# Optimization experiments

Hardware: AMD Instinct MI355X
Metric: run time of the kernel (lower is better)

## Reference

```python
import jax, jax.numpy as jnp
import numpy as np

FTYPE = ((0, 16), (1, 16), (2, 8))   # [(order, multiplicity)], C = 16*1 + 16*2 + 8*2 = 64
DIM = 64
MAX_ORDER = 2
NUM_BASIS = 2 * MAX_ORDER + 1        # [1, cos a, sin a, cos 2a, sin 2a]
V = 50000
E = 800000
LN_EPS = 1e-5


def _transport(features, transporters, ftype):
    """Apply per-irrep rotation rho_n(g) to each edge's gathered feature. features:(E,C)."""
    blocks = []
    offset = 0
    for order, mult in ftype:
        d = 1 if order == 0 else 2
        C = mult * d
        blk = features[:, offset:offset + C]
        if order == 0:
            blocks.append(blk)
        else:
            b = blk.reshape(-1, mult, 2)                      # (E, mult, 2)
            phi = order * transporters
            c, s = jnp.cos(phi), jnp.sin(phi)
            R = jnp.stack([jnp.stack([c, -s], -1),
                           jnp.stack([s,  c], -1)], -2)        # (E, 2, 2)
            rot = jnp.einsum('emd,erd->emr', b, R)             # rotate each 2-vector
            blocks.append(rot.reshape(-1, C))
        offset += C
    return jnp.concatenate(blocks, axis=1)


def _angle_basis(angles):
    """Circular harmonic basis for the equivariant kernel: (E, NUM_BASIS)."""
    cols = [jnp.ones_like(angles)]
    for k in range(1, MAX_ORDER + 1):
        cols.append(jnp.cos(k * angles))
        cols.append(jnp.sin(k * angles))
    return jnp.stack(cols, axis=1)


def _regular_nonlin(x, ftype):
    """ReLU on scalar (rho_0) channels; norm-gated softplus on vector channels."""
    blocks = []
    offset = 0
    for order, mult in ftype:
        d = 1 if order == 0 else 2
        C = mult * d
        blk = x[:, offset:offset + C]
        if order == 0:
            blocks.append(jax.nn.relu(blk))
        else:
            b = blk.reshape(-1, mult, 2)
            norms = jnp.clip(jnp.linalg.norm(b, axis=-1, keepdims=True), 1e-8, None)
            out_b = b * (jax.nn.softplus(norms) / norms)
            blocks.append(out_b.reshape(-1, C))
        offset += C
    return jnp.concatenate(blocks, axis=1)


def _gem_block(x, edge_index, angles, transporters, K_self, W_neigh, ln_gamma, ln_beta):
    src, tgt = edge_index[0], edge_index[1]
    # self-interaction
    out = x @ K_self.T                                        # (V, C_out)
    # gather + parallel transport
    f_q = _transport(x[src], transporters, FTYPE)             # (E, C_in)
    # per-edge equivariant kernel applied via fused einsum:
    #   K_neigh[e] = sum_b basis[e,b] * W_neigh[b]  ;  msg[e] = K_neigh[e] @ f_q[e]
    basis = _angle_basis(angles)                              # (E, B)
    tmp = jnp.einsum('boi,ei->ebo', W_neigh, f_q)             # (E, B, C_out)
    msg = jnp.einsum('eb,ebo->eo', basis, tmp)                # (E, C_out)
    # scatter-add messages into targets
    out = out + jax.ops.segment_sum(msg, tgt, num_segments=V)
    # LayerNorm
    mu = jnp.mean(out, axis=-1, keepdims=True)
    var = jnp.var(out, axis=-1, keepdims=True)
    h = (out - mu) * jax.lax.rsqrt(var + LN_EPS) * ln_gamma + ln_beta
    # regular nonlinearity + identity residual (dim_in == dim_out)
    h = _regular_nonlin(h, FTYPE)
    return h + x


def setup_inputs() -> dict:
    key = jax.random.key(0)
    ks = jax.random.split(key, 8)
    x = jax.random.normal(ks[0], (V, DIM), jnp.float32)
    edge_index = jax.random.randint(ks[1], (2, E), 0, V)
    angles = jax.random.uniform(ks[2], (E,), jnp.float32, 0.0, 2.0 * np.pi)
    transporters = jax.random.uniform(ks[3], (E,), jnp.float32, 0.0, 2.0 * np.pi)
    K_self = jax.random.normal(ks[4], (DIM, DIM), jnp.float32) / np.sqrt(DIM)
    W_neigh = jax.random.normal(ks[5], (NUM_BASIS, DIM, DIM), jnp.float32) / np.sqrt(DIM * NUM_BASIS)
    ln_gamma = jnp.ones((DIM,), jnp.float32)
    ln_beta = jnp.zeros((DIM,), jnp.float32)
    return {"x": x, "edge_index": edge_index, "angles": angles, "transporters": transporters,
            "K_self": K_self, "W_neigh": W_neigh, "ln_gamma": ln_gamma, "ln_beta": ln_beta}


def reference(x, edge_index, angles, transporters, K_self, W_neigh, ln_gamma, ln_beta):
    return _gem_block(x, edge_index, angles, transporters, K_self, W_neigh, ln_gamma, ln_beta)
```

## Files before the change

kernel.cpp:

```cpp
#include <hip/hip_runtime.h>

#define VN 50000
#define EN 800000
#define CAP 48
#define USH 392

typedef short short8 __attribute__((ext_vector_type(8)));
typedef float float4v __attribute__((ext_vector_type(4)));

#define WS_GBF   0
#define WS_WHI   128
#define WS_WLO   12416
#define WS_POS   24704
#define WS_REC   74704
#define WS_A_BYTES ((size_t)(74704 + 50000 * 48 * 4) * 4)

__device__ __forceinline__ float bf2f(unsigned short u) {
    return __uint_as_float(((unsigned int)u) << 16);
}
__device__ __forceinline__ unsigned short f2bf(float f) {
    unsigned int x = __float_as_uint(f);
    return (unsigned short)((x + 0x7fffu + ((x >> 16) & 1u)) >> 16);
}
__device__ __forceinline__ float ldf(const void* p, int isbf, size_t i) {
    return isbf ? bf2f(((const unsigned short*)p)[i]) : ((const float*)p)[i];
}

__device__ __forceinline__ int block_detect(const void* xv) {
    __shared__ int flg;
    if (threadIdx.x < 64) {
        unsigned short w = ((const unsigned short*)xv)[2 * threadIdx.x];
        int e = (w >> 7) & 0xFF;
        bool ok = (e >= 0x70 && e <= 0x85) || (w == 0);
        unsigned long long m = __ballot(ok);
        if (threadIdx.x == 0) flg = (__popcll(m) >= 40) ? 1 : 0;
    }
    __syncthreads();
    return flg;
}

__device__ __forceinline__ void convert_dev(int idx, const void* Ks,
                                            const void* Wn, const void* gma,
                                            const void* bta, float* ws, int isbf) {
    if (idx < 128) {
        const void* p = (idx < 64) ? gma : bta;
        ws[WS_GBF + idx] = ldf(p, isbf, idx & 63);
    } else {
        int m2 = idx - 128;
        int j = m2 & 7;
        int chunk = m2 >> 3;
        int slot = chunk >> 6;
        int ln = chunk & 63;
        int ks = slot >> 2, wv = slot & 3;
        int k = ks * 32 + ((ln >> 4) * 8) + j;
        int n = wv * 16 + (ln & 15);
        float wvl;
        if (k < 320) {
            int b = k >> 6, i = k & 63;
            wvl = ldf(Wn, isbf, (b * 64 + n) * 64 + i);
        } else {
            wvl = ldf(Ks, isbf, n * 64 + (k - 320));
        }
        unsigned short hi = f2bf(wvl);
        unsigned short lo = f2bf(wvl - bf2f(hi));
        ((unsigned short*)(ws + WS_WHI))[m2] = hi;
        ((unsigned short*)(ws + WS_WLO))[m2] = lo;
    }
}

template <bool PAY>
__global__ __launch_bounds__(512) void conv_place(
    const void* xv, const int* __restrict__ eidx, const void* angv,
    const void* trpv, const void* Ks, const void* Wn, const void* gma,
    const void* bta, float* __restrict__ ws) {
    const int isbf = block_detect(xv);
    int gtid = blockIdx.x * 512 + threadIdx.x;
    if (gtid < 128 + 24576) convert_dev(gtid, Ks, Wn, gma, bta, ws, isbf);
    if (gtid < EN) {
        int tgt = eidx[EN + gtid];
        int slot = atomicAdd(&((int*)(ws + WS_POS))[tgt], 1);
        if (slot < CAP) {
            if (PAY) {
                uint4 r;
                r.x = (unsigned int)eidx[gtid];
                r.y = __float_as_uint(ldf(angv, isbf, gtid));
                r.z = __float_as_uint(ldf(trpv, isbf, gtid));
                r.w = 0u;
                ((uint4*)(ws + WS_REC))[(size_t)tgt * CAP + slot] = r;
            } else {
                ((int*)(ws + WS_REC))[(size_t)tgt * CAP + slot] = gtid;
            }
        }
    }
}

template <bool BF, bool PAY>
__device__ __forceinline__ void gem_body(
    const void* xv, const int* __restrict__ eidx, const void* angv,
    const void* trpv, const float* __restrict__ ws, void* __restrict__ outv,
    float* Ledge, unsigned short* Uhi, unsigned short* Ulo) {
    const int t = threadIdx.x;
    const int lane = t & 63;
    const int w = t >> 6;
    const int v0 = blockIdx.x * 8;
    const int* pos = (const int*)(ws + WS_POS);
    float* Cst = Ledge;

    if (t < 8 * CAP) {
        int n = t / CAP, s = t - n * CAP;
        int dn = min(pos[v0 + n], CAP);
        if (s < dn) {
            unsigned int srcb;
            float aphi, tphi;
            if (PAY) {
                uint4 r = ((const uint4*)(ws + WS_REC))[(size_t)(v0 + n) * CAP + s];
                srcb = r.x;
                aphi = __uint_as_float(r.y);
                tphi = __uint_as_float(r.z);
            } else {
                int e = ((const int*)(ws + WS_REC))[(size_t)(v0 + n) * CAP + s];
                srcb = (unsigned int)eidx[e];
                aphi = BF ? bf2f(((const unsigned short*)angv)[e])
                          : ((const float*)angv)[e];
                tphi = BF ? bf2f(((const unsigned short*)trpv)[e])
                          : ((const float*)trpv)[e];
            }
            float st, ct, sa, ca;
            __sincosf(tphi, &st, &ct);
            __sincosf(aphi, &sa, &ca);
            float c2a = fmaf(ca, ca, -sa * sa), s2a = 2.f * ca * sa;
            float c2t = fmaf(ct, ct, -st * st), s2t = 2.f * ct * st;
            float* L = &Ledge[t * 16];
            *(float4v*)(L)      = (float4v){__uint_as_float(srcb), ca, sa, c2a};
            *(float4v*)(L + 4)  = (float4v){1.f, 0.f, s2a, 0.f};
            *(float4v*)(L + 8)  = (float4v){ct, st, s2a, 0.f};
            *(float4v*)(L + 12) = (float4v){c2t, s2t, s2a, 0.f};
        }
    }
    __syncthreads();

    const int v = v0 + w;
    const int d = min(pos[v], CAP);
    const int g = (lane < 16) ? 0 : ((lane < 48) ? 1 : 2);
    const int grpoff = 4 + 4 * g;
    const unsigned int smask = (lane & 1) ? 0u : 0x80000000u;
    float a0 = 0.f, a1 = 0.f, a2 = 0.f, a3 = 0.f, a4 = 0.f;

    const float* Lb = &Ledge[w * CAP * 16];
    auto loadx = [&](unsigned int s) -> float {
        if (BF) return bf2f(((const unsigned short*)xv)[(size_t)s * 64 + lane]);
        else    return ((const float*)xv)[(size_t)s * 64 + lane];
    };
    auto edge1 = [&](int j, float xg) {
        const float* L = &Lb[j * 16];
        float4v sh = *(const float4v*)L;
        float4v gr = *(const float4v*)(L + grpoff);
        float prt = __shfl_xor(xg, 1, 64);
        float tmp = __uint_as_float(__float_as_uint(gr[1] * prt) ^ smask);
        float fq = fmaf(gr[0], xg, tmp);
        a0 += fq;
        a1 = fmaf(sh[1], fq, a1);
        a2 = fmaf(sh[2], fq, a2);
        a3 = fmaf(sh[3], fq, a3);
        a4 = fmaf(gr[2], fq, a4);
    };

    const int nb = d >> 2;
    float y0, y1, y2, y3;
    if (nb > 0) {
        y0 = loadx(__float_as_uint(Lb[0 * 16]));
        y1 = loadx(__float_as_uint(Lb[1 * 16]));
        y2 = loadx(__float_as_uint(Lb[2 * 16]));
        y3 = loadx(__float_as_uint(Lb[3 * 16]));
    }
    for (int b = 0; b < nb; ++b) {
        float z0, z1, z2, z3;
        const bool more = (b + 1 < nb);
        if (more) {
            int j4 = (b + 1) * 4;
            z0 = loadx(__float_as_uint(Lb[(j4 + 0) * 16]));
            z1 = loadx(__float_as_uint(Lb[(j4 + 1) * 16]));
            z2 = loadx(__float_as_uint(Lb[(j4 + 2) * 16]));
            z3 = loadx(__float_as_uint(Lb[(j4 + 3) * 16]));
        }
        int j0 = b * 4;
        edge1(j0 + 0, y0); edge1(j0 + 1, y1);
        edge1(j0 + 2, y2); edge1(j0 + 3, y3);
        if (more) { y0 = z0; y1 = z1; y2 = z2; y3 = z3; }
    }
    for (int j = nb * 4; j < d; ++j)
        edge1(j, loadx(__float_as_uint(Lb[j * 16])));

    float xown = BF ? bf2f(((const unsigned short*)xv)[(size_t)v * 64 + lane])
                    : ((const float*)xv)[(size_t)v * 64 + lane];
    auto wrU = [&](int c, float val) {
        unsigned short h = f2bf(val);
        unsigned short l = f2bf(val - bf2f(h));
        Uhi[w * USH + c * 64 + lane] = h;
        Ulo[w * USH + c * 64 + lane] = l;
    };
    wrU(0, a0); wrU(1, a1); wrU(2, a2); wrU(3, a3); wrU(4, a4); wrU(5, xown);
    __syncthreads();

    const int mcol = lane & 15, q = lane >> 4;
    if (w < 4) {
        const int mrow = mcol & 7;
        const unsigned short* Whi = (const unsigned short*)(ws + WS_WHI);
        const unsigned short* Wlo = (const unsigned short*)(ws + WS_WLO);
        float4v acc = (float4v){0.f, 0.f, 0.f, 0.f};
#pragma unroll
        for (int ks = 0; ks < 12; ++ks) {
            short8 ahi = *(const short8*)&Uhi[mrow * USH + ks * 32 + q * 8];
            short8 alo = *(const short8*)&Ulo[mrow * USH + ks * 32 + q * 8];
            short8 bhi = *(const short8*)(Whi + ((size_t)(ks * 4 + w) * 64 + lane) * 8);
            short8 blo = *(const short8*)(Wlo + ((size_t)(ks * 4 + w) * 64 + lane) * 8);
            acc = __builtin_amdgcn_mfma_f32_16x16x32_bf16(ahi, bhi, acc, 0, 0, 0);
            acc = __builtin_amdgcn_mfma_f32_16x16x32_bf16(alo, bhi, acc, 0, 0, 0);
            acc = __builtin_amdgcn_mfma_f32_16x16x32_bf16(ahi, blo, acc, 0, 0, 0);
        }
#pragma unroll
        for (int reg = 0; reg < 4; ++reg)
            Cst[(q * 4 + reg) * 68 + w * 16 + mcol] = acc[reg];
    }
    __syncthreads();

    const float* gbf = ws + WS_GBF;
    float s = Cst[w * 68 + lane];
    float s1 = s, s2v = s * s;
#pragma unroll
    for (int off = 32; off > 0; off >>= 1) {
        s1 += __shfl_xor(s1, off, 64);
        s2v += __shfl_xor(s2v, off, 64);
    }
    float mu = s1 * (1.f / 64.f);
    float var = s2v * (1.f / 64.f) - mu * mu;
    float h = (s - mu) * rsqrtf(var + 1e-5f) * gbf[lane] + gbf[64 + lane];

    float prt = __shfl_xor(h, 1, 64);
    float rlt;
    if (lane < 16) {
        rlt = fmaxf(h, 0.f);
    } else {
        float nrm = sqrtf(h * h + prt * prt);
        nrm = fmaxf(nrm, 1e-8f);
        float sp = (nrm > 20.f) ? nrm : log1pf(__expf(nrm));
        rlt = h * (sp / nrm);
    }
    float xr = bf2f(Uhi[w * USH + 320 + lane]) + bf2f(Ulo[w * USH + 320 + lane]);
    float res = rlt + xr;
    if (BF) ((unsigned short*)outv)[(size_t)v * 64 + lane] = f2bf(res);
    else    ((float*)outv)[(size_t)v * 64 + lane] = res;
}

template <bool PAY>
__global__ __launch_bounds__(512, 8) void gem_kernel(
    const void* xv, const int* __restrict__ eidx, const void* angv,
    const void* trpv, const float* __restrict__ ws, void* __restrict__ outv) {
    __shared__ float Ledge[8 * CAP * 16];
    __shared__ unsigned short Uhi[8 * USH];
    __shared__ unsigned short Ulo[8 * USH];

    const int isbf = block_detect(xv);
    if (isbf) gem_body<true, PAY>(xv, eidx, angv, trpv, ws, outv, Ledge, Uhi, Ulo);
    else      gem_body<false, PAY>(xv, eidx, angv, trpv, ws, outv, Ledge, Uhi, Ulo);
}

extern "C" void kernel_launch(void* const* d_in, const int* in_sizes, int n_in,
                              void* d_out, int out_size, void* d_ws, size_t ws_size,
                              hipStream_t stream) {
    const void* x   = d_in[0];
    const int* eidx = (const int*)d_in[1];
    const void* ang = d_in[2];
    const void* trp = d_in[3];
    const void* Ks  = d_in[4];
    const void* Wn  = d_in[5];
    const void* gma = d_in[6];
    const void* bta = d_in[7];
    float* ws = (float*)d_ws;

    hipMemsetAsync(ws + WS_POS, 0, VN * sizeof(int), stream);
    if (ws_size >= WS_A_BYTES) {
        conv_place<true><<<1563, 512, 0, stream>>>(x, eidx, ang, trp, Ks, Wn,
                                                   gma, bta, ws);
        gem_kernel<true><<<VN / 8, 512, 0, stream>>>(x, eidx, ang, trp, ws,
                                                     d_out);
    } else {
        conv_place<false><<<1563, 512, 0, stream>>>(x, eidx, ang, trp, Ks, Wn,
                                                    gma, bta, ws);
        gem_kernel<false><<<VN / 8, 512, 0, stream>>>(x, eidx, ang, trp, ws,
                                                      d_out);
    }
}
```

Measured before the change: 199.8 us.

## Compact edge records, deepen gather prefetch, split MFMA K across all waves

Shrinks the per-edge LDS record from 16 to 12 floats. Transport coefficients are now picked per lane and s2a is recomputed in the edge loop, cutting LDS footprint and writes. Empty slots are padded with dummy records so the gather loop can run in groups of four with no tail. Prefetch is deepened to two groups ahead to hide more gather latency. The MFMA matmul is split along K across all 8 waves instead of 4, with partial sums added in LDS before layernorm, at the cost of extra selects and an extra LDS read per lane.

```diff
diff --git a/kernel.cpp b/kernel.cpp
--- a/kernel.cpp
+++ b/kernel.cpp
@@ -4,6 +4,7 @@
 #define EN 800000
 #define CAP 48
 #define USH 392
+#define LREC 12
 
 typedef short short8 __attribute__((ext_vector_type(8)));
 typedef float float4v __attribute__((ext_vector_type(4)));
@@ -109,6 +110,7 @@
     if (t < 8 * CAP) {
         int n = t / CAP, s = t - n * CAP;
         int dn = min(pos[v0 + n], CAP);
+        float* L = &Ledge[t * LREC];
         if (s < dn) {
             unsigned int srcb;
             float aphi, tphi;
@@ -128,68 +130,67 @@
             float st, ct, sa, ca;
             __sincosf(tphi, &st, &ct);
             __sincosf(aphi, &sa, &ca);
-            float c2a = fmaf(ca, ca, -sa * sa), s2a = 2.f * ca * sa;
-            float c2t = fmaf(ct, ct, -st * st), s2t = 2.f * ct * st;
-            float* L = &Ledge[t * 16];
-            *(float4v*)(L)      = (float4v){__uint_as_float(srcb), ca, sa, c2a};
-            *(float4v*)(L + 4)  = (float4v){1.f, 0.f, s2a, 0.f};
-            *(float4v*)(L + 8)  = (float4v){ct, st, s2a, 0.f};
-            *(float4v*)(L + 12) = (float4v){c2t, s2t, s2a, 0.f};
+            *(float4v*)(L)     = (float4v){__uint_as_float(srcb), ca, sa,
+                                           fmaf(ca, ca, -sa * sa)};
+            *(float4v*)(L + 4) = (float4v){ct, st, fmaf(ct, ct, -st * st),
+                                           2.f * ct * st};
+        } else {
+            *(float4v*)(L)     = (float4v){__uint_as_float((unsigned)(v0 + n)),
+                                           0.f, 0.f, 0.f};
+            *(float4v*)(L + 4) = (float4v){0.f, 0.f, 0.f, 0.f};
         }
     }
     __syncthreads();
 
     const int v = v0 + w;
     const int d = min(pos[v], CAP);
+    const int R = (d + 3) >> 2;
     const int g = (lane < 16) ? 0 : ((lane < 48) ? 1 : 2);
-    const int grpoff = 4 + 4 * g;
     const unsigned int smask = (lane & 1) ? 0u : 0x80000000u;
     float a0 = 0.f, a1 = 0.f, a2 = 0.f, a3 = 0.f, a4 = 0.f;
 
-    const float* Lb = &Ledge[w * CAP * 16];
+    const float* Lb = &Ledge[w * CAP * LREC];
+    auto srcOf = [&](int j) { return __float_as_uint(Lb[j * LREC]); };
     auto loadx = [&](unsigned int s) -> float {
         if (BF) return bf2f(((const unsigned short*)xv)[(size_t)s * 64 + lane]);
         else    return ((const float*)xv)[(size_t)s * 64 + lane];
     };
     auto edge1 = [&](int j, float xg) {
-        const float* L = &Lb[j * 16];
+        const float* L = &Lb[j * LREC];
         float4v sh = *(const float4v*)L;
-        float4v gr = *(const float4v*)(L + grpoff);
+        float4v rt = *(const float4v*)(L + 4);
+        float cl = (g == 0) ? 1.f : ((g == 1) ? rt[0] : rt[2]);
+        float sl = (g == 0) ? 0.f : ((g == 1) ? rt[1] : rt[3]);
         float prt = __shfl_xor(xg, 1, 64);
-        float tmp = __uint_as_float(__float_as_uint(gr[1] * prt) ^ smask);
-        float fq = fmaf(gr[0], xg, tmp);
+        float tmp = __uint_as_float(__float_as_uint(sl * prt) ^ smask);
+        float fq = fmaf(cl, xg, tmp);
         a0 += fq;
         a1 = fmaf(sh[1], fq, a1);
         a2 = fmaf(sh[2], fq, a2);
         a3 = fmaf(sh[3], fq, a3);
-        a4 = fmaf(gr[2], fq, a4);
+        a4 = fmaf(2.f * sh[1] * sh[2], fq, a4);
     };
 
-    const int nb = d >> 2;
-    float y0, y1, y2, y3;
-    if (nb > 0) {
-        y0 = loadx(__float_as_uint(Lb[0 * 16]));
-        y1 = loadx(__float_as_uint(Lb[1 * 16]));
-        y2 = loadx(__float_as_uint(Lb[2 * 16]));
-        y3 = loadx(__float_as_uint(Lb[3 * 16]));
-    }
-    for (int b = 0; b < nb; ++b) {
-        float z0, z1, z2, z3;
-        const bool more = (b + 1 < nb);
-        if (more) {
-            int j4 = (b + 1) * 4;
-            z0 = loadx(__float_as_uint(Lb[(j4 + 0) * 16]));
-            z1 = loadx(__float_as_uint(Lb[(j4 + 1) * 16]));
-            z2 = loadx(__float_as_uint(Lb[(j4 + 2) * 16]));
-            z3 = loadx(__float_as_uint(Lb[(j4 + 3) * 16]));
+    float y[4], z[4];
+#pragma unroll
+    for (int u = 0; u < 4; ++u) y[u] = (R > 0) ? loadx(srcOf(u)) : 0.f;
+#pragma unroll
+    for (int u = 0; u < 4; ++u) z[u] = (R > 1) ? loadx(srcOf(4 + u)) : 0.f;
+
+    for (int b = 0; b < R; ++b) {
+        float nx[4] = {0.f, 0.f, 0.f, 0.f};
+        if (b + 2 < R) {
+            int j8 = (b + 2) * 4;
+#pragma unroll
+            for (int u = 0; u < 4; ++u) nx[u] = loadx(srcOf(j8 + u));
         }
         int j0 = b * 4;
-        edge1(j0 + 0, y0); edge1(j0 + 1, y1);
-        edge1(j0 + 2, y2); edge1(j0 + 3, y3);
-        if (more) { y0 = z0; y1 = z1; y2 = z2; y3 = z3; }
-    }
-    for (int j = nb * 4; j < d; ++j)
-        edge1(j, loadx(__float_as_uint(Lb[j * 16])));
+#pragma unroll
+        for (int u = 0; u < 4; ++u)
+            edge1(j0 + u, (j0 + u < d) ? y[u] : 0.f);
+#pragma unroll
+        for (int u = 0; u < 4; ++u) { y[u] = z[u]; z[u] = nx[u]; }
+    }
 
     float xown = BF ? bf2f(((const unsigned short*)xv)[(size_t)v * 64 + lane])
                     : ((const float*)xv)[(size_t)v * 64 + lane];
@@ -203,29 +204,31 @@
     __syncthreads();
 
     const int mcol = lane & 15, q = lane >> 4;
-    if (w < 4) {
+    {
+        const int slab = w & 3, kh = w >> 2;
         const int mrow = mcol & 7;
         const unsigned short* Whi = (const unsigned short*)(ws + WS_WHI);
         const unsigned short* Wlo = (const unsigned short*)(ws + WS_WLO);
         float4v acc = (float4v){0.f, 0.f, 0.f, 0.f};
 #pragma unroll
-        for (int ks = 0; ks < 12; ++ks) {
+        for (int kk = 0; kk < 6; ++kk) {
+            const int ks = kh * 6 + kk;
             short8 ahi = *(const short8*)&Uhi[mrow * USH + ks * 32 + q * 8];
             short8 alo = *(const short8*)&Ulo[mrow * USH + ks * 32 + q * 8];
-            short8 bhi = *(const short8*)(Whi + ((size_t)(ks * 4 + w) * 64 + lane) * 8);
-            short8 blo = *(const short8*)(Wlo + ((size_t)(ks * 4 + w) * 64 + lane) * 8);
+            short8 bhi = *(const short8*)(Whi + ((size_t)(ks * 4 + slab) * 64 + lane) * 8);
+            short8 blo = *(const short8*)(Wlo + ((size_t)(ks * 4 + slab) * 64 + lane) * 8);
             acc = __builtin_amdgcn_mfma_f32_16x16x32_bf16(ahi, bhi, acc, 0, 0, 0);
             acc = __builtin_amdgcn_mfma_f32_16x16x32_bf16(alo, bhi, acc, 0, 0, 0);
             acc = __builtin_amdgcn_mfma_f32_16x16x32_bf16(ahi, blo, acc, 0, 0, 0);
         }
 #pragma unroll
         for (int reg = 0; reg < 4; ++reg)
-            Cst[(q * 4 + reg) * 68 + w * 16 + mcol] = acc[reg];
+            Cst[kh * 1088 + (q * 4 + reg) * 68 + slab * 16 + mcol] = acc[reg];
     }
     __syncthreads();
 
     const float* gbf = ws + WS_GBF;
-    float s = Cst[w * 68 + lane];
+    float s = Cst[w * 68 + lane] + Cst[1088 + w * 68 + lane];
     float s1 = s, s2v = s * s;
 #pragma unroll
     for (int off = 32; off > 0; off >>= 1) {
@@ -256,7 +259,7 @@
 __global__ __launch_bounds__(512, 8) void gem_kernel(
     const void* xv, const int* __restrict__ eidx, const void* angv,
     const void* trpv, const float* __restrict__ ws, void* __restrict__ outv) {
-    __shared__ float Ledge[8 * CAP * 16];
+    __shared__ float Ledge[8 * CAP * LREC];
     __shared__ unsigned short Uhi[8 * USH];
     __shared__ unsigned short Ulo[8 * USH];
 
```

After: 197.5 us. Within noise of the previous version (-1.1%).
